# Performance work log

Measured on AMD Instinct MI355X. Metric: run time of the kernel, lower is better.

The kernel has to match this reference:

```python
import jax, jax.numpy as jnp
import numpy as np

B, T, C = 2, 2048, 2048
N_HEAD = 16
N_KV = 4
HEAD = C // N_HEAD  # 128
GROUP = N_HEAD // N_KV


def setup_inputs() -> dict:
    key = jax.random.key(0)
    ks = jax.random.split(key, 5)
    s = 1.0 / np.sqrt(C)
    return {
        "x": jax.random.normal(ks[0], (B, T, C), dtype=jnp.float32),
        "Wq": jax.random.normal(ks[1], (C, C), dtype=jnp.float32) * s,
        "Wk": jax.random.normal(ks[2], (C, N_KV * HEAD), dtype=jnp.float32) * s,
        "Wv": jax.random.normal(ks[3], (C, N_KV * HEAD), dtype=jnp.float32) * s,
        "Wo": jax.random.normal(ks[4], (C, C), dtype=jnp.float32) * s,
    }


def reference(x, Wq, Wk, Wv, Wo):
    Bx, Tx, Cx = x.shape
    q = (x @ Wq).reshape(Bx, Tx, N_HEAD, HEAD).transpose(0, 2, 1, 3)  # (B,H,T,D)
    k = (x @ Wk).reshape(Bx, Tx, N_KV, HEAD).transpose(0, 2, 1, 3)    # (B,KV,T,D)
    v = (x @ Wv).reshape(Bx, Tx, N_KV, HEAD).transpose(0, 2, 1, 3)
    # expand kv heads to query heads (GQA): repeat each kv head GROUP times
    k = jnp.repeat(k, GROUP, axis=1)  # (B,H,T,D)
    v = jnp.repeat(v, GROUP, axis=1)
    scale = 1.0 / np.sqrt(HEAD).astype(np.float32)
    att = jnp.einsum("bhqd,bhkd->bhqk", q, k) * scale  # (B,H,T,T)
    causal = jnp.tril(jnp.ones((Tx, Tx), dtype=bool))
    att = jnp.where(causal[None, None], att, -jnp.inf)
    att = jax.nn.softmax(att, axis=-1)
    y = jnp.einsum("bhqk,bhkd->bhqd", att, v)  # (B,H,T,D)
    y = y.transpose(0, 2, 1, 3).reshape(Bx, Tx, Cx)
    return y @ Wo
```

## Files before the change

kernel.cpp:

```cpp
#include <hip/hip_runtime.h>
#include <cstdint>

typedef unsigned short u16;
typedef unsigned int u32;
typedef __attribute__((ext_vector_type(8))) __bf16 bf16x8;
typedef __attribute__((ext_vector_type(4))) float f32x4;
typedef __attribute__((ext_vector_type(4))) unsigned short u16x4;

#define AS1 __attribute__((address_space(1)))
#define AS3 __attribute__((address_space(3)))

__device__ __forceinline__ void gload16(const void* g, void* l) {
    __builtin_amdgcn_global_load_lds((AS1 void*)g, (AS3 void*)l, 16, 0, 0);
}

__device__ __forceinline__ u16 f2bf(float f) {
    u32 u = __builtin_bit_cast(u32, f);
    u = (u + 0x7fffu + ((u >> 16) & 1u)) >> 16;
    return (u16)u;
}

__device__ __forceinline__ void store_c(u16* p, float v)   { *p = f2bf(v); }
__device__ __forceinline__ void store_c(float* p, float v) { *p = v; }

__global__ void cvt_bf16(const float* __restrict__ in, u16* __restrict__ out) {
    int i = (blockIdx.x * blockDim.x + threadIdx.x) * 4;
    float4 v = *(const float4*)(in + i);
    u16x4 o = { f2bf(v.x), f2bf(v.y), f2bf(v.z), f2bf(v.w) };
    *(u16x4*)(out + i) = o;
}

__global__ void transpose_cvt(const float* __restrict__ in, u16* __restrict__ out,
                              int R, int Ccols)
{
    __shared__ float tile[32][33];
    int c0 = blockIdx.x * 32, r0 = blockIdx.y * 32;
    int tx = threadIdx.x, ty = threadIdx.y;
#pragma unroll
    for (int i = 0; i < 32; i += 8)
        tile[ty + i][tx] = in[(size_t)(r0 + ty + i) * Ccols + c0 + tx];
    __syncthreads();
#pragma unroll
    for (int i = 0; i < 32; i += 8)
        out[(size_t)(c0 + ty + i) * R + r0 + tx] = f2bf(tile[tx][ty + i]);
}

__global__ void vtrans(const u16* __restrict__ QKV, u16* __restrict__ VT) {
    __shared__ u16 tile[32][33];
    int b = blockIdx.z;
    int c0 = blockIdx.x * 32, r0 = blockIdx.y * 32;
    int tx = threadIdx.x, ty = threadIdx.y;
#pragma unroll
    for (int i = 0; i < 32; i += 8)
        tile[ty + i][tx] = QKV[(size_t)(b * 2048 + r0 + ty + i) * 3072 + 2560 + c0 + tx];
    __syncthreads();
#pragma unroll
    for (int i = 0; i < 32; i += 8)
        VT[(size_t)(b * 512 + c0 + ty + i) * 2048 + r0 + tx] = tile[tx][ty + i];
}

template <typename OT>
__global__ __launch_bounds__(256, 2) void gemm_bt(
    const u16* __restrict__ A, const u16* __restrict__ Bt,
    OT* __restrict__ C, int M, int N, int K)
{
    __shared__ u16 As[128 * 64];
    __shared__ u16 Bs[128 * 64];
    const int tid  = threadIdx.x;
    const int wave = tid >> 6, lane = tid & 63;
    const int quad = lane >> 4, l15 = lane & 15;
    const int bm0 = blockIdx.y * 128, bn0 = blockIdx.x * 128;
    const int wr = (wave >> 1) * 64, wc = (wave & 1) * 64;

    const f32x4 zero = {0.f, 0.f, 0.f, 0.f};
    f32x4 acc[4][4];
#pragma unroll
    for (int i = 0; i < 4; ++i)
#pragma unroll
        for (int j = 0; j < 4; ++j) acc[i][j] = zero;

    const int srow = lane >> 3;
    const int jsw  = ((lane & 7) ^ srow) * 8;

    for (int k0 = 0; k0 < K; k0 += 64) {
#pragma unroll
        for (int i = 0; i < 4; ++i) {
            int c = wave * 4 + i;
            gload16(A  + (size_t)(bm0 + c * 8 + srow) * K + k0 + jsw, As + c * 512);
            gload16(Bt + (size_t)(bn0 + c * 8 + srow) * K + k0 + jsw, Bs + c * 512);
        }
        __syncthreads();
#pragma unroll
        for (int ks = 0; ks < 2; ++ks) {
            bf16x8 a[4], b[4];
#pragma unroll
            for (int t = 0; t < 4; ++t) {
                int rd = ((ks * 4 + quad) ^ (l15 & 7)) * 8;
                a[t] = *(const bf16x8*)(As + (wr + t * 16 + l15) * 64 + rd);
                b[t] = *(const bf16x8*)(Bs + (wc + t * 16 + l15) * 64 + rd);
            }
#pragma unroll
            for (int i = 0; i < 4; ++i)
#pragma unroll
                for (int j = 0; j < 4; ++j)
                    acc[i][j] = __builtin_amdgcn_mfma_f32_16x16x32_bf16(a[i], b[j], acc[i][j], 0, 0, 0);
        }
        __syncthreads();
    }
#pragma unroll
    for (int i = 0; i < 4; ++i) {
        int grow = bm0 + wr + i * 16 + quad * 4;
#pragma unroll
        for (int j = 0; j < 4; ++j) {
            int gcol = bn0 + wc + j * 16 + l15;
#pragma unroll
            for (int r = 0; r < 4; ++r)
                store_c(&C[(size_t)(grow + r) * N + gcol], acc[i][j][r]);
        }
    }
}

__device__ __forceinline__ void pv_step(
    f32x4 (&s)[4], f32x4 (&o)[9], bool diag,
    const u16* Vsc, u16* pw, const bf16x8 ones,
    int quad, int l15, int wave)
{
    const float c1 = 0.12752817f;
    const float c2 = 28.85390082f;
#pragma unroll
    for (int kc = 0; kc < 4; ++kc)
#pragma unroll
        for (int r = 0; r < 4; ++r) {
            float arg = fmaf(s[kc][r], c1, -c2);
            if (diag && (kc * 16 + l15) > (wave * 16 + quad * 4 + r)) arg = -10000.f;
            float p = __builtin_amdgcn_exp2f(arg);
            pw[(quad * 4 + r) * 80 + kc * 16 + l15] = f2bf(p);
        }
    asm volatile("" ::: "memory");
#pragma unroll
    for (int ks2 = 0; ks2 < 2; ++ks2) {
        bf16x8 pa = *(const bf16x8*)(pw + l15 * 80 + ks2 * 32 + quad * 8);
#pragma unroll
        for (int d = 0; d < 8; ++d) {
            bf16x8 bv = *(const bf16x8*)(Vsc + (d * 16 + l15) * 64 + (((ks2 * 4 + quad) ^ (l15 & 7)) * 8));
            o[d] = __builtin_amdgcn_mfma_f32_16x16x32_bf16(pa, bv, o[d], 0, 0, 0);
        }
        o[8] = __builtin_amdgcn_mfma_f32_16x16x32_bf16(pa, ones, o[8], 0, 0, 0);
    }
    asm volatile("" ::: "memory");
}

__global__ __launch_bounds__(256, 2) void attn(
    const u16* __restrict__ QKV, const u16* __restrict__ VT, u16* __restrict__ Y)
{
    __shared__ u16 Ks[2][64 * 128];
    __shared__ u16 Vs[2][128 * 64];
    __shared__ u16 Ps[4][16 * 80];

    const int tid  = threadIdx.x;
    const int wave = tid >> 6, lane = tid & 63;
    const int quad = lane >> 4, l15 = lane & 15;
    const int pi = blockIdx.x;
    const int qtA = pi, qtB = 31 - pi;
    const int bh = blockIdx.y;
    const int b = bh >> 4, h = bh & 15, kv = h >> 2;

    const int q0A = qtA * 64 + wave * 16;
    const int q0B = qtB * 64 + wave * 16;

    bf16x8 aqA[4], aqB[4];
    {
        const u16* qpA = QKV + (size_t)(b * 2048 + q0A + l15) * 3072 + h * 128 + quad * 8;
        const u16* qpB = QKV + (size_t)(b * 2048 + q0B + l15) * 3072 + h * 128 + quad * 8;
#pragma unroll
        for (int ks = 0; ks < 4; ++ks) {
            aqA[ks] = *(const bf16x8*)(qpA + ks * 32);
            aqB[ks] = *(const bf16x8*)(qpB + ks * 32);
        }
    }

    bf16x8 ones;
#pragma unroll
    for (int i = 0; i < 8; ++i) ones[i] = __builtin_bit_cast(__bf16, (u16)0x3F80);

    const f32x4 zero = {0.f, 0.f, 0.f, 0.f};
    f32x4 oA[9], oB[9];
#pragma unroll
    for (int i = 0; i < 9; ++i) { oA[i] = zero; oB[i] = zero; }

    const u16* Kbase = QKV + 2048 + kv * 128;
    const u16* Vbase = VT + (size_t)((b * 4 + kv) * 128) * 2048;
    u16* pw = &Ps[wave][0];

    const int kr = lane >> 4;
    const int vr = lane >> 3;
    const int vjs = ((lane & 7) ^ vr) * 8;

    auto stage = [&](int buf, int kt) {
#pragma unroll
        for (int i = 0; i < 4; ++i) {
            int ci = wave * 4 + i;
            int krow = ci * 4 + kr;
            int kjs = ((lane & 15) ^ (krow & 15)) * 8;
            gload16(Kbase + (size_t)(b * 2048 + kt * 64 + krow) * 3072 + kjs,
                    &Ks[buf][ci * 512]);
            int vrow = ci * 8 + vr;
            gload16(Vbase + (size_t)vrow * 2048 + kt * 64 + vjs, &Vs[buf][ci * 512]);
        }
    };

    stage(0, 0);
    __syncthreads();

    for (int kt = 0; kt <= qtB; ++kt) {
        const int cur = kt & 1;
        if (kt < qtB) stage(cur ^ 1, kt + 1);

        const bool aA = (kt <= qtA);
        const u16* Ksc = &Ks[cur][0];
        const u16* Vsc = &Vs[cur][0];

        f32x4 sA[4], sB[4];
#pragma unroll
        for (int i = 0; i < 4; ++i) { sA[i] = zero; sB[i] = zero; }
#pragma unroll
        for (int ks = 0; ks < 4; ++ks)
#pragma unroll
            for (int kc = 0; kc < 4; ++kc) {
                bf16x8 bk = *(const bf16x8*)(Ksc + (kc * 16 + l15) * 128 + (((ks * 4 + quad) ^ l15) * 8));
                if (aA) sA[kc] = __builtin_amdgcn_mfma_f32_16x16x32_bf16(aqA[ks], bk, sA[kc], 0, 0, 0);
                sB[kc] = __builtin_amdgcn_mfma_f32_16x16x32_bf16(aqB[ks], bk, sB[kc], 0, 0, 0);
            }

        if (aA) pv_step(sA, oA, kt == qtA, Vsc, pw, ones, quad, l15, wave);
        pv_step(sB, oB, kt == qtB, Vsc, pw, ones, quad, l15, wave);

        __syncthreads();
    }

    float invA[4], invB[4];
#pragma unroll
    for (int r = 0; r < 4; ++r) { invA[r] = 1.0f / oA[8][r]; invB[r] = 1.0f / oB[8][r]; }
#pragma unroll
    for (int d = 0; d < 8; ++d)
#pragma unroll
        for (int r = 0; r < 4; ++r) {
            Y[(size_t)(b * 2048 + q0A + quad * 4 + r) * 2048 + h * 128 + d * 16 + l15] =
                f2bf(oA[d][r] * invA[r]);
            Y[(size_t)(b * 2048 + q0B + quad * 4 + r) * 2048 + h * 128 + d * 16 + l15] =
                f2bf(oB[d][r] * invB[r]);
        }
}

extern "C" void kernel_launch(void* const* d_in, const int* in_sizes, int n_in,
                              void* d_out, int out_size, void* d_ws, size_t ws_size,
                              hipStream_t stream)
{
    const float* x  = (const float*)d_in[0];
    const float* Wq = (const float*)d_in[1];
    const float* Wk = (const float*)d_in[2];
    const float* Wv = (const float*)d_in[3];
    const float* Wo = (const float*)d_in[4];
    float* out = (float*)d_out;

    char* ws = (char*)d_ws;
    u16* xb    = (u16*)ws; ws += (size_t)4096 * 2048 * 2;
    u16* WqkvT = (u16*)ws; ws += (size_t)3072 * 2048 * 2;
    u16* WoT   = (u16*)ws; ws += (size_t)2048 * 2048 * 2;
    u16* QKVb  = (u16*)ws; ws += (size_t)4096 * 3072 * 2;
    u16* VT    = (u16*)ws;
    u16* Y     = xb;

    dim3 tblk(32, 8, 1);
    cvt_bf16<<<8192, 256, 0, stream>>>(x, xb);
    transpose_cvt<<<dim3(64, 64, 1), tblk, 0, stream>>>(Wq, WqkvT, 2048, 2048);
    transpose_cvt<<<dim3(16, 64, 1), tblk, 0, stream>>>(Wk, WqkvT + (size_t)2048 * 2048, 2048, 512);
    transpose_cvt<<<dim3(16, 64, 1), tblk, 0, stream>>>(Wv, WqkvT + (size_t)2560 * 2048, 2048, 512);
    transpose_cvt<<<dim3(64, 64, 1), tblk, 0, stream>>>(Wo, WoT, 2048, 2048);

    gemm_bt<u16><<<dim3(24, 32, 1), 256, 0, stream>>>(xb, WqkvT, QKVb, 4096, 3072, 2048);

    vtrans<<<dim3(16, 64, 2), tblk, 0, stream>>>(QKVb, VT);

    attn<<<dim3(16, 32, 1), 256, 0, stream>>>(QKVb, VT, Y);

    gemm_bt<float><<<dim3(16, 32, 1), 256, 0, stream>>>(Y, WoT, out, 4096, 2048, 2048);
}
```

Baseline: 285.7 us.

## Split paired query tiles across eight waves and single-buffer V

The attention kernel now runs 512 threads per block. Waves 0-3 handle query tile A and waves 4-7 handle tile B, instead of each wave handling both, so per-wave register pressure drops and more waves are available for latency hiding. V is now single-buffered and loaded inside each iteration, with an extra barrier between the QK/softmax phase and the PV phase. Separately, the bf16 conversion now uses the compiler's native cast. The trade-off is an extra barrier per iteration, V load latency that is no longer prefetched, and idle A-waves once their tile is finished.

```diff
diff --git a/kernel.cpp b/kernel.cpp
--- a/kernel.cpp
+++ b/kernel.cpp
@@ -15,9 +15,7 @@
 }
 
 __device__ __forceinline__ u16 f2bf(float f) {
-    u32 u = __builtin_bit_cast(u32, f);
-    u = (u + 0x7fffu + ((u >> 16) & 1u)) >> 16;
-    return (u16)u;
+    return __builtin_bit_cast(u16, (__bf16)f);
 }
 
 __device__ __forceinline__ void store_c(u16* p, float v)   { *p = f2bf(v); }
@@ -120,63 +118,30 @@
     }
 }
 
-__device__ __forceinline__ void pv_step(
-    f32x4 (&s)[4], f32x4 (&o)[9], bool diag,
-    const u16* Vsc, u16* pw, const bf16x8 ones,
-    int quad, int l15, int wave)
-{
-    const float c1 = 0.12752817f;
-    const float c2 = 28.85390082f;
-#pragma unroll
-    for (int kc = 0; kc < 4; ++kc)
-#pragma unroll
-        for (int r = 0; r < 4; ++r) {
-            float arg = fmaf(s[kc][r], c1, -c2);
-            if (diag && (kc * 16 + l15) > (wave * 16 + quad * 4 + r)) arg = -10000.f;
-            float p = __builtin_amdgcn_exp2f(arg);
-            pw[(quad * 4 + r) * 80 + kc * 16 + l15] = f2bf(p);
-        }
-    asm volatile("" ::: "memory");
-#pragma unroll
-    for (int ks2 = 0; ks2 < 2; ++ks2) {
-        bf16x8 pa = *(const bf16x8*)(pw + l15 * 80 + ks2 * 32 + quad * 8);
-#pragma unroll
-        for (int d = 0; d < 8; ++d) {
-            bf16x8 bv = *(const bf16x8*)(Vsc + (d * 16 + l15) * 64 + (((ks2 * 4 + quad) ^ (l15 & 7)) * 8));
-            o[d] = __builtin_amdgcn_mfma_f32_16x16x32_bf16(pa, bv, o[d], 0, 0, 0);
-        }
-        o[8] = __builtin_amdgcn_mfma_f32_16x16x32_bf16(pa, ones, o[8], 0, 0, 0);
-    }
-    asm volatile("" ::: "memory");
-}
-
-__global__ __launch_bounds__(256, 2) void attn(
+__global__ __launch_bounds__(512, 4) void attn(
     const u16* __restrict__ QKV, const u16* __restrict__ VT, u16* __restrict__ Y)
 {
     __shared__ u16 Ks[2][64 * 128];
-    __shared__ u16 Vs[2][128 * 64];
-    __shared__ u16 Ps[4][16 * 80];
+    __shared__ u16 Vs[128 * 64];
+    __shared__ u16 Ps[8][16 * 80];
 
     const int tid  = threadIdx.x;
     const int wave = tid >> 6, lane = tid & 63;
     const int quad = lane >> 4, l15 = lane & 15;
+    const int w4 = wave & 3;
     const int pi = blockIdx.x;
     const int qtA = pi, qtB = 31 - pi;
     const int bh = blockIdx.y;
     const int b = bh >> 4, h = bh & 15, kv = h >> 2;
 
-    const int q0A = qtA * 64 + wave * 16;
-    const int q0B = qtB * 64 + wave * 16;
-
-    bf16x8 aqA[4], aqB[4];
+    const int myqt = (wave < 4) ? qtA : qtB;
+    const int q0 = myqt * 64 + w4 * 16;
+
+    bf16x8 aq[4];
     {
-        const u16* qpA = QKV + (size_t)(b * 2048 + q0A + l15) * 3072 + h * 128 + quad * 8;
-        const u16* qpB = QKV + (size_t)(b * 2048 + q0B + l15) * 3072 + h * 128 + quad * 8;
-#pragma unroll
-        for (int ks = 0; ks < 4; ++ks) {
-            aqA[ks] = *(const bf16x8*)(qpA + ks * 32);
-            aqB[ks] = *(const bf16x8*)(qpB + ks * 32);
-        }
+        const u16* qp = QKV + (size_t)(b * 2048 + q0 + l15) * 3072 + h * 128 + quad * 8;
+#pragma unroll
+        for (int ks = 0; ks < 4; ++ks) aq[ks] = *(const bf16x8*)(qp + ks * 32);
     }
 
     bf16x8 ones;
@@ -184,9 +149,9 @@
     for (int i = 0; i < 8; ++i) ones[i] = __builtin_bit_cast(__bf16, (u16)0x3F80);
 
     const f32x4 zero = {0.f, 0.f, 0.f, 0.f};
-    f32x4 oA[9], oB[9];
-#pragma unroll
-    for (int i = 0; i < 9; ++i) { oA[i] = zero; oB[i] = zero; }
+    f32x4 o[9];
+#pragma unroll
+    for (int i = 0; i < 9; ++i) o[i] = zero;
 
     const u16* Kbase = QKV + 2048 + kv * 128;
     const u16* Vbase = VT + (size_t)((b * 4 + kv) * 128) * 2048;
@@ -196,60 +161,90 @@
     const int vr = lane >> 3;
     const int vjs = ((lane & 7) ^ vr) * 8;
 
-    auto stage = [&](int buf, int kt) {
-#pragma unroll
-        for (int i = 0; i < 4; ++i) {
-            int ci = wave * 4 + i;
+    auto stageK = [&](int buf, int kt) {
+#pragma unroll
+        for (int i = 0; i < 2; ++i) {
+            int ci = wave * 2 + i;
             int krow = ci * 4 + kr;
             int kjs = ((lane & 15) ^ (krow & 15)) * 8;
             gload16(Kbase + (size_t)(b * 2048 + kt * 64 + krow) * 3072 + kjs,
                     &Ks[buf][ci * 512]);
+        }
+    };
+    auto stageV = [&](int kt) {
+#pragma unroll
+        for (int i = 0; i < 2; ++i) {
+            int ci = wave * 2 + i;
             int vrow = ci * 8 + vr;
-            gload16(Vbase + (size_t)vrow * 2048 + kt * 64 + vjs, &Vs[buf][ci * 512]);
+            gload16(Vbase + (size_t)vrow * 2048 + kt * 64 + vjs, &Vs[ci * 512]);
         }
     };
 
-    stage(0, 0);
+    const float c1 = 0.12752817f;
+    const float c2 = 28.85390082f;
+
+    stageK(0, 0);
     __syncthreads();
 
     for (int kt = 0; kt <= qtB; ++kt) {
         const int cur = kt & 1;
-        if (kt < qtB) stage(cur ^ 1, kt + 1);
-
-        const bool aA = (kt <= qtA);
+        stageV(kt);
+        if (kt < qtB) stageK(cur ^ 1, kt + 1);
+
+        const bool act = (kt <= myqt);
         const u16* Ksc = &Ks[cur][0];
-        const u16* Vsc = &Vs[cur][0];
-
-        f32x4 sA[4], sB[4];
-#pragma unroll
-        for (int i = 0; i < 4; ++i) { sA[i] = zero; sB[i] = zero; }
-#pragma unroll
-        for (int ks = 0; ks < 4; ++ks)
-#pragma unroll
-            for (int kc = 0; kc < 4; ++kc) {
-                bf16x8 bk = *(const bf16x8*)(Ksc + (kc * 16 + l15) * 128 + (((ks * 4 + quad) ^ l15) * 8));
-                if (aA) sA[kc] = __builtin_amdgcn_mfma_f32_16x16x32_bf16(aqA[ks], bk, sA[kc], 0, 0, 0);
-                sB[kc] = __builtin_amdgcn_mfma_f32_16x16x32_bf16(aqB[ks], bk, sB[kc], 0, 0, 0);
+
+        if (act) {
+            f32x4 s[4];
+#pragma unroll
+            for (int i = 0; i < 4; ++i) s[i] = zero;
+#pragma unroll
+            for (int ks = 0; ks < 4; ++ks)
+#pragma unroll
+                for (int kc = 0; kc < 4; ++kc) {
+                    bf16x8 bk = *(const bf16x8*)(Ksc + (kc * 16 + l15) * 128 + (((ks * 4 + quad) ^ l15) * 8));
+                    s[kc] = __builtin_amdgcn_mfma_f32_16x16x32_bf16(aq[ks], bk, s[kc], 0, 0, 0);
+                }
+            const bool diag = (kt == myqt);
+#pragma unroll
+            for (int kc = 0; kc < 4; ++kc)
+#pragma unroll
+                for (int r = 0; r < 4; ++r) {
+                    float arg = fmaf(s[kc][r], c1, -c2);
+                    if (diag && (kc * 16 + l15) > (w4 * 16 + quad * 4 + r)) arg = -10000.f;
+                    float p = __builtin_amdgcn_exp2f(arg);
+                    pw[(quad * 4 + r) * 80 + kc * 16 + l15] = f2bf(p);
+                }
+            asm volatile("" ::: "memory");
+        }
+
+        __syncthreads();
+
+        if (act) {
+#pragma unroll
+            for (int ks2 = 0; ks2 < 2; ++ks2) {
+                bf16x8 pa = *(const bf16x8*)(pw + l15 * 80 + ks2 * 32 + quad * 8);
+#pragma unroll
+                for (int d = 0; d < 8; ++d) {
+                    bf16x8 bv = *(const bf16x8*)(Vs + (d * 16 + l15) * 64 + (((ks2 * 4 + quad) ^ (l15 & 7)) * 8));
+                    o[d] = __builtin_amdgcn_mfma_f32_16x16x32_bf16(pa, bv, o[d], 0, 0, 0);
+                }
+                o[8] = __builtin_amdgcn_mfma_f32_16x16x32_bf16(pa, ones, o[8], 0, 0, 0);
             }
-
-        if (aA) pv_step(sA, oA, kt == qtA, Vsc, pw, ones, quad, l15, wave);
-        pv_step(sB, oB, kt == qtB, Vsc, pw, ones, quad, l15, wave);
-
-        __syncthreads();
-    }
-
-    float invA[4], invB[4];
-#pragma unroll
-    for (int r = 0; r < 4; ++r) { invA[r] = 1.0f / oA[8][r]; invB[r] = 1.0f / oB[8][r]; }
+        }
+
+        __syncthreads();
+    }
+
+    float inv[4];
+#pragma unroll
+    for (int r = 0; r < 4; ++r) inv[r] = 1.0f / o[8][r];
 #pragma unroll
     for (int d = 0; d < 8; ++d)
 #pragma unroll
-        for (int r = 0; r < 4; ++r) {
-            Y[(size_t)(b * 2048 + q0A + quad * 4 + r) * 2048 + h * 128 + d * 16 + l15] =
-                f2bf(oA[d][r] * invA[r]);
-            Y[(size_t)(b * 2048 + q0B + quad * 4 + r) * 2048 + h * 128 + d * 16 + l15] =
-                f2bf(oB[d][r] * invB[r]);
-        }
+        for (int r = 0; r < 4; ++r)
+            Y[(size_t)(b * 2048 + q0 + quad * 4 + r) * 2048 + h * 128 + d * 16 + l15] =
+                f2bf(o[d][r] * inv[r]);
 }
 
 extern "C" void kernel_launch(void* const* d_in, const int* in_sizes, int n_in,
@@ -282,7 +277,7 @@
 
     vtrans<<<dim3(16, 64, 2), tblk, 0, stream>>>(QKVb, VT);
 
-    attn<<<dim3(16, 32, 1), 256, 0, stream>>>(QKVb, VT, Y);
+    attn<<<dim3(16, 32, 1), 512, 0, stream>>>(QKVb, VT, Y);
 
     gemm_bt<float><<<dim3(16, 32, 1), 256, 0, stream>>>(Y, WoT, out, 4096, 2048, 2048);
 }
```

New measurement: 271.9 us. -4.8%, faster.

## Split attention q-tiles across waves and fuse weight/input prep kernels

Applied to the files above, without the earlier changes.

The attention kernel now gives waves 0-1 the short query tile and waves 2-3 the long one, each wave handling 32 rows. Previously every wave handled 16 rows of both tiles. Waves on the short tile skip compute once past their diagonal, which removes the per-step branch on tile A but leaves two waves idle at the barrier for the rest of the loop. The five conversion and transpose launches are merged into one prep kernel to cut launch overhead, and f2bf now uses the native bf16 conversion.

```diff
diff --git a/kernel.cpp b/kernel.cpp
--- a/kernel.cpp
+++ b/kernel.cpp
@@ -15,34 +15,41 @@
 }
 
 __device__ __forceinline__ u16 f2bf(float f) {
-    u32 u = __builtin_bit_cast(u32, f);
-    u = (u + 0x7fffu + ((u >> 16) & 1u)) >> 16;
-    return (u16)u;
+    return __builtin_bit_cast(u16, (__bf16)f);
 }
 
 __device__ __forceinline__ void store_c(u16* p, float v)   { *p = f2bf(v); }
 __device__ __forceinline__ void store_c(float* p, float v) { *p = v; }
 
-__global__ void cvt_bf16(const float* __restrict__ in, u16* __restrict__ out) {
-    int i = (blockIdx.x * blockDim.x + threadIdx.x) * 4;
-    float4 v = *(const float4*)(in + i);
-    u16x4 o = { f2bf(v.x), f2bf(v.y), f2bf(v.z), f2bf(v.w) };
-    *(u16x4*)(out + i) = o;
-}
-
-__global__ void transpose_cvt(const float* __restrict__ in, u16* __restrict__ out,
-                              int R, int Ccols)
-{
+__global__ void prep(const float* __restrict__ x,
+                     const float* __restrict__ Wq, const float* __restrict__ Wk,
+                     const float* __restrict__ Wv, const float* __restrict__ Wo,
+                     u16* __restrict__ xb, u16* __restrict__ Wt)
+{
+    const int bid = blockIdx.x;
+    if (bid >= 10240) {
+        int tid = threadIdx.y * 32 + threadIdx.x;
+        size_t i = ((size_t)(bid - 10240) * 256 + tid) * 4;
+        float4 v = *(const float4*)(x + i);
+        u16x4 o = { f2bf(v.x), f2bf(v.y), f2bf(v.z), f2bf(v.w) };
+        *(u16x4*)(xb + i) = o;
+        return;
+    }
+    const float* src; u16* dst; int C, bx, by;
+    if (bid < 4096)      { src = Wq; dst = Wt;                          C = 2048; bx = bid & 63; by = bid >> 6; }
+    else if (bid < 5120) { src = Wk; dst = Wt + (size_t)2048 * 2048;    C = 512;  int i = bid - 4096; bx = i & 15; by = i >> 4; }
+    else if (bid < 6144) { src = Wv; dst = Wt + (size_t)2560 * 2048;    C = 512;  int i = bid - 5120; bx = i & 15; by = i >> 4; }
+    else                 { src = Wo; dst = Wt + (size_t)3072 * 2048;    C = 2048; int i = bid - 6144; bx = i & 63; by = i >> 6; }
     __shared__ float tile[32][33];
-    int c0 = blockIdx.x * 32, r0 = blockIdx.y * 32;
+    int c0 = bx * 32, r0 = by * 32;
     int tx = threadIdx.x, ty = threadIdx.y;
 #pragma unroll
     for (int i = 0; i < 32; i += 8)
-        tile[ty + i][tx] = in[(size_t)(r0 + ty + i) * Ccols + c0 + tx];
+        tile[ty + i][tx] = src[(size_t)(r0 + ty + i) * C + c0 + tx];
     __syncthreads();
 #pragma unroll
     for (int i = 0; i < 32; i += 8)
-        out[(size_t)(c0 + ty + i) * R + r0 + tx] = f2bf(tile[tx][ty + i]);
+        dst[(size_t)(c0 + ty + i) * 2048 + r0 + tx] = f2bf(tile[tx][ty + i]);
 }
 
 __global__ void vtrans(const u16* __restrict__ QKV, u16* __restrict__ VT) {
@@ -120,36 +127,6 @@
     }
 }
 
-__device__ __forceinline__ void pv_step(
-    f32x4 (&s)[4], f32x4 (&o)[9], bool diag,
-    const u16* Vsc, u16* pw, const bf16x8 ones,
-    int quad, int l15, int wave)
-{
-    const float c1 = 0.12752817f;
-    const float c2 = 28.85390082f;
-#pragma unroll
-    for (int kc = 0; kc < 4; ++kc)
-#pragma unroll
-        for (int r = 0; r < 4; ++r) {
-            float arg = fmaf(s[kc][r], c1, -c2);
-            if (diag && (kc * 16 + l15) > (wave * 16 + quad * 4 + r)) arg = -10000.f;
-            float p = __builtin_amdgcn_exp2f(arg);
-            pw[(quad * 4 + r) * 80 + kc * 16 + l15] = f2bf(p);
-        }
-    asm volatile("" ::: "memory");
-#pragma unroll
-    for (int ks2 = 0; ks2 < 2; ++ks2) {
-        bf16x8 pa = *(const bf16x8*)(pw + l15 * 80 + ks2 * 32 + quad * 8);
-#pragma unroll
-        for (int d = 0; d < 8; ++d) {
-            bf16x8 bv = *(const bf16x8*)(Vsc + (d * 16 + l15) * 64 + (((ks2 * 4 + quad) ^ (l15 & 7)) * 8));
-            o[d] = __builtin_amdgcn_mfma_f32_16x16x32_bf16(pa, bv, o[d], 0, 0, 0);
-        }
-        o[8] = __builtin_amdgcn_mfma_f32_16x16x32_bf16(pa, ones, o[8], 0, 0, 0);
-    }
-    asm volatile("" ::: "memory");
-}
-
 __global__ __launch_bounds__(256, 2) void attn(
     const u16* __restrict__ QKV, const u16* __restrict__ VT, u16* __restrict__ Y)
 {
@@ -165,18 +142,16 @@
     const int bh = blockIdx.y;
     const int b = bh >> 4, h = bh & 15, kv = h >> 2;
 
-    const int q0A = qtA * 64 + wave * 16;
-    const int q0B = qtB * 64 + wave * 16;
-
-    bf16x8 aqA[4], aqB[4];
-    {
-        const u16* qpA = QKV + (size_t)(b * 2048 + q0A + l15) * 3072 + h * 128 + quad * 8;
-        const u16* qpB = QKV + (size_t)(b * 2048 + q0B + l15) * 3072 + h * 128 + quad * 8;
-#pragma unroll
-        for (int ks = 0; ks < 4; ++ks) {
-            aqA[ks] = *(const bf16x8*)(qpA + ks * 32);
-            aqB[ks] = *(const bf16x8*)(qpB + ks * 32);
-        }
+    const int myqt = (wave < 2) ? qtA : qtB;
+    const int qbase = (wave & 1) * 32;
+    const int q0 = myqt * 64 + qbase;
+
+    bf16x8 aq[2][4];
+#pragma unroll
+    for (int mt = 0; mt < 2; ++mt) {
+        const u16* qp = QKV + (size_t)(b * 2048 + q0 + mt * 16 + l15) * 3072 + h * 128 + quad * 8;
+#pragma unroll
+        for (int ks = 0; ks < 4; ++ks) aq[mt][ks] = *(const bf16x8*)(qp + ks * 32);
     }
 
     bf16x8 ones;
@@ -184,9 +159,13 @@
     for (int i = 0; i < 8; ++i) ones[i] = __builtin_bit_cast(__bf16, (u16)0x3F80);
 
     const f32x4 zero = {0.f, 0.f, 0.f, 0.f};
-    f32x4 oA[9], oB[9];
-#pragma unroll
-    for (int i = 0; i < 9; ++i) { oA[i] = zero; oB[i] = zero; }
+    f32x4 o[2][8], o8[2];
+#pragma unroll
+    for (int mt = 0; mt < 2; ++mt) {
+#pragma unroll
+        for (int i = 0; i < 8; ++i) o[mt][i] = zero;
+        o8[mt] = zero;
+    }
 
     const u16* Kbase = QKV + 2048 + kv * 128;
     const u16* Vbase = VT + (size_t)((b * 4 + kv) * 128) * 2048;
@@ -209,6 +188,9 @@
         }
     };
 
+    const float c1 = 0.12752817f;
+    const float c2 = 28.85390082f;
+
     stage(0, 0);
     __syncthreads();
 
@@ -216,40 +198,66 @@
         const int cur = kt & 1;
         if (kt < qtB) stage(cur ^ 1, kt + 1);
 
-        const bool aA = (kt <= qtA);
-        const u16* Ksc = &Ks[cur][0];
-        const u16* Vsc = &Vs[cur][0];
-
-        f32x4 sA[4], sB[4];
-#pragma unroll
-        for (int i = 0; i < 4; ++i) { sA[i] = zero; sB[i] = zero; }
-#pragma unroll
-        for (int ks = 0; ks < 4; ++ks)
-#pragma unroll
-            for (int kc = 0; kc < 4; ++kc) {
-                bf16x8 bk = *(const bf16x8*)(Ksc + (kc * 16 + l15) * 128 + (((ks * 4 + quad) ^ l15) * 8));
-                if (aA) sA[kc] = __builtin_amdgcn_mfma_f32_16x16x32_bf16(aqA[ks], bk, sA[kc], 0, 0, 0);
-                sB[kc] = __builtin_amdgcn_mfma_f32_16x16x32_bf16(aqB[ks], bk, sB[kc], 0, 0, 0);
+        if (kt <= myqt) {
+            const u16* Ksc = &Ks[cur][0];
+            const u16* Vsc = &Vs[cur][0];
+
+            f32x4 s[2][4];
+#pragma unroll
+            for (int mt = 0; mt < 2; ++mt)
+#pragma unroll
+                for (int i = 0; i < 4; ++i) s[mt][i] = zero;
+#pragma unroll
+            for (int ks = 0; ks < 4; ++ks)
+#pragma unroll
+                for (int kc = 0; kc < 4; ++kc) {
+                    bf16x8 bk = *(const bf16x8*)(Ksc + (kc * 16 + l15) * 128 + (((ks * 4 + quad) ^ l15) * 8));
+                    s[0][kc] = __builtin_amdgcn_mfma_f32_16x16x32_bf16(aq[0][ks], bk, s[0][kc], 0, 0, 0);
+                    s[1][kc] = __builtin_amdgcn_mfma_f32_16x16x32_bf16(aq[1][ks], bk, s[1][kc], 0, 0, 0);
+                }
+            const bool diag = (kt == myqt);
+
+#pragma unroll
+            for (int mt = 0; mt < 2; ++mt) {
+#pragma unroll
+                for (int kc = 0; kc < 4; ++kc)
+#pragma unroll
+                    for (int r = 0; r < 4; ++r) {
+                        float arg = fmaf(s[mt][kc][r], c1, -c2);
+                        if (diag && (kc * 16 + l15) > (qbase + mt * 16 + quad * 4 + r)) arg = -10000.f;
+                        float p = __builtin_amdgcn_exp2f(arg);
+                        pw[(quad * 4 + r) * 80 + kc * 16 + l15] = f2bf(p);
+                    }
+                asm volatile("" ::: "memory");
+#pragma unroll
+                for (int ks2 = 0; ks2 < 2; ++ks2) {
+                    bf16x8 pa = *(const bf16x8*)(pw + l15 * 80 + ks2 * 32 + quad * 8);
+#pragma unroll
+                    for (int d = 0; d < 8; ++d) {
+                        bf16x8 bv = *(const bf16x8*)(Vsc + (d * 16 + l15) * 64 + (((ks2 * 4 + quad) ^ (l15 & 7)) * 8));
+                        o[mt][d] = __builtin_amdgcn_mfma_f32_16x16x32_bf16(pa, bv, o[mt][d], 0, 0, 0);
+                    }
+                    o8[mt] = __builtin_amdgcn_mfma_f32_16x16x32_bf16(pa, ones, o8[mt], 0, 0, 0);
+                }
+                asm volatile("" ::: "memory");
             }
-
-        if (aA) pv_step(sA, oA, kt == qtA, Vsc, pw, ones, quad, l15, wave);
-        pv_step(sB, oB, kt == qtB, Vsc, pw, ones, quad, l15, wave);
+        }
 
         __syncthreads();
     }
 
-    float invA[4], invB[4];
-#pragma unroll
-    for (int r = 0; r < 4; ++r) { invA[r] = 1.0f / oA[8][r]; invB[r] = 1.0f / oB[8][r]; }
-#pragma unroll
-    for (int d = 0; d < 8; ++d)
-#pragma unroll
-        for (int r = 0; r < 4; ++r) {
-            Y[(size_t)(b * 2048 + q0A + quad * 4 + r) * 2048 + h * 128 + d * 16 + l15] =
-                f2bf(oA[d][r] * invA[r]);
-            Y[(size_t)(b * 2048 + q0B + quad * 4 + r) * 2048 + h * 128 + d * 16 + l15] =
-                f2bf(oB[d][r] * invB[r]);
-        }
+#pragma unroll
+    for (int mt = 0; mt < 2; ++mt) {
+        float inv[4];
+#pragma unroll
+        for (int r = 0; r < 4; ++r) inv[r] = 1.0f / o8[mt][r];
+#pragma unroll
+        for (int d = 0; d < 8; ++d)
+#pragma unroll
+            for (int r = 0; r < 4; ++r)
+                Y[(size_t)(b * 2048 + q0 + mt * 16 + quad * 4 + r) * 2048 + h * 128 + d * 16 + l15] =
+                    f2bf(o[mt][d][r] * inv[r]);
+    }
 }
 
 extern "C" void kernel_launch(void* const* d_in, const int* in_sizes, int n_in,
@@ -264,23 +272,18 @@
     float* out = (float*)d_out;
 
     char* ws = (char*)d_ws;
-    u16* xb    = (u16*)ws; ws += (size_t)4096 * 2048 * 2;
-    u16* WqkvT = (u16*)ws; ws += (size_t)3072 * 2048 * 2;
-    u16* WoT   = (u16*)ws; ws += (size_t)2048 * 2048 * 2;
-    u16* QKVb  = (u16*)ws; ws += (size_t)4096 * 3072 * 2;
-    u16* VT    = (u16*)ws;
-    u16* Y     = xb;
-
-    dim3 tblk(32, 8, 1);
-    cvt_bf16<<<8192, 256, 0, stream>>>(x, xb);
-    transpose_cvt<<<dim3(64, 64, 1), tblk, 0, stream>>>(Wq, WqkvT, 2048, 2048);
-    transpose_cvt<<<dim3(16, 64, 1), tblk, 0, stream>>>(Wk, WqkvT + (size_t)2048 * 2048, 2048, 512);
-    transpose_cvt<<<dim3(16, 64, 1), tblk, 0, stream>>>(Wv, WqkvT + (size_t)2560 * 2048, 2048, 512);
-    transpose_cvt<<<dim3(64, 64, 1), tblk, 0, stream>>>(Wo, WoT, 2048, 2048);
-
-    gemm_bt<u16><<<dim3(24, 32, 1), 256, 0, stream>>>(xb, WqkvT, QKVb, 4096, 3072, 2048);
-
-    vtrans<<<dim3(16, 64, 2), tblk, 0, stream>>>(QKVb, VT);
+    u16* xb   = (u16*)ws; ws += (size_t)4096 * 2048 * 2;
+    u16* Wt   = (u16*)ws; ws += (size_t)5120 * 2048 * 2;
+    u16* QKVb = (u16*)ws; ws += (size_t)4096 * 3072 * 2;
+    u16* VT   = (u16*)ws;
+    u16* Y    = xb;
+    u16* WoT  = Wt + (size_t)3072 * 2048;
+
+    prep<<<18432, dim3(32, 8, 1), 0, stream>>>(x, Wq, Wk, Wv, Wo, xb, Wt);
+
+    gemm_bt<u16><<<dim3(24, 32, 1), 256, 0, stream>>>(xb, Wt, QKVb, 4096, 3072, 2048);
+
+    vtrans<<<dim3(16, 64, 2), dim3(32, 8, 1), 0, stream>>>(QKVb, VT);
 
     attn<<<dim3(16, 32, 1), 256, 0, stream>>>(QKVb, VT, Y);
 
```

Measured after the change: 283.9 us. About the same (-0.6%).
